# Kernel optimization log

Measured on AMD Instinct MI355X. Metric: run time of the kernel, lower is better.

## Reference

```python
import jax, jax.numpy as jnp
import numpy as np

B, T, D, V, M, K = 16, 4096, 512, 32000, 256, 3
OPERATOR_RANK = 8
COVERAGE_FLOOR = 0.05
LN_EPS = 1e-5


def _causal_conv(h, w, b):
    # h: [B,T,D] -> NCH layout, left-pad K-1 for causality (matches F.pad((pad,0)))
    x = h.transpose(0, 2, 1)
    k = w.shape[-1]
    y = jax.lax.conv_general_dilated(x, w, (1,), [(k - 1, 0)],
                                     dimension_numbers=('NCH', 'OIH', 'NCH'))
    return (y + b[None, :, None]).transpose(0, 2, 1)


def _layernorm(x, g, b):
    mu = x.mean(-1, keepdims=True)
    var = ((x - mu) ** 2).mean(-1, keepdims=True)
    return (x - mu) * jax.lax.rsqrt(var + LN_EPS) * g + b


def _masked_median(vals, mask):
    # torch .median() on n valid elems = sorted[(n-1)//2] (lower median)
    valid = mask > 0.5
    cnt = valid.sum(-1)  # [B]
    s = jnp.sort(jnp.where(valid, vals, jnp.inf), axis=-1)
    idx = jnp.maximum((cnt - 1) // 2, 0).astype(jnp.int32)
    med = jnp.take_along_axis(s, idx[:, None], axis=-1)  # [B,1]
    return jnp.where(cnt[:, None] > 0, med, 0.0)


def setup_inputs() -> dict:
    key = jax.random.key(0)
    ks = jax.random.split(key, 10)
    return {
        'prompt_content_units': jax.random.randint(ks[0], (B, T), 0, V),
        'prompt_duration_obs': jax.random.uniform(ks[1], (B, T), minval=0.01, maxval=1.0),
        'prompt_mask': (jax.random.uniform(ks[2], (B, T)) < 0.9).astype(jnp.float32),
        'emb': jax.random.normal(ks[3], (V, D)) * 0.02,
        'proj_w': jax.random.normal(ks[4], (D, 4)) * 0.1,
        'proj_b': jnp.zeros((D,)),
        'conv1_w': jax.random.normal(ks[5], (D, D, K)) * 0.02,
        'conv1_b': jnp.zeros((D,)),
        'conv2_w': jax.random.normal(ks[6], (D, D, K)) * 0.02,
        'conv2_b': jnp.zeros((D,)),
        'ln_g': jnp.ones((D,)),
        'ln_b': jnp.zeros((D,)),
        'role_key': jax.random.normal(ks[7], (M, D)) * 0.02,
    }


def reference(prompt_content_units, prompt_duration_obs, prompt_mask,
              emb, proj_w, proj_b, conv1_w, conv1_b, conv2_w, conv2_b,
              ln_g, ln_b, role_key):
    mask = jnp.clip(prompt_mask, 0.0, 1.0)                       # [B,T]
    logdur = jnp.log(jnp.maximum(prompt_duration_obs, 1e-4)) * mask
    z = jnp.zeros_like(logdur)
    aux = jnp.stack([logdur, z, z, z], axis=-1)                  # [B,T,4]
    hidden = emb[prompt_content_units] + aux @ proj_w.T + proj_b # [B,T,D]
    hidden = jax.nn.gelu(_causal_conv(hidden, conv1_w, conv1_b), approximate=False)
    hidden = jax.nn.gelu(_causal_conv(hidden, conv2_w, conv2_b), approximate=False)
    hidden = _layernorm(hidden, ln_g, ln_b) * mask[..., None]

    score = jnp.einsum('btd,md->btm', hidden, role_key) / jnp.sqrt(jnp.float32(D))
    score = jnp.where(mask[..., None] <= 0.0, -10000.0, score)
    attn = jax.nn.softmax(score, axis=-1) * mask[..., None]      # [B,T,M]

    support = jnp.maximum(mask.sum(1, keepdims=True), 1.0)       # [B,1]
    global_rate = _masked_median(logdur, mask)                   # [B,1]
    ref_residual = (logdur - global_rate) * mask                 # [B,T]

    coverage = jnp.maximum(attn.sum(1), 1e-6)                    # [B,M]
    role_value = jnp.einsum('btm,bt->bm', attn, ref_residual) / coverage
    diff2 = (ref_residual[..., None] - role_value[:, None, :]) ** 2
    role_var = jnp.maximum((attn * diff2).sum(1) / coverage, 1e-4)
    role_cov = jnp.maximum(coverage / support, COVERAGE_FLOOR)
    prompt_role_fit = jnp.einsum('btm,bm->bt', attn, role_value) * mask
    zero_operator = jnp.zeros((mask.shape[0], OPERATOR_RANK), dtype=prompt_duration_obs.dtype)

    return (global_rate, zero_operator, role_value, role_var, role_cov,
            mask, logdur, ref_residual, attn, prompt_role_fit)
```

## Files before the change

### kernel.cpp

```cpp
#include <hip/hip_runtime.h>
#include <math.h>
#include <stdint.h>

#define B_  16
#define T_  4096
#define D_  512
#define M_  256
#define TP_ 4098

static constexpr long O_RATE = 0;
static constexpr long O_ZOP  = 16;
static constexpr long O_RVAL = 144;
static constexpr long O_RVAR = 4240;
static constexpr long O_RCOV = 8336;
static constexpr long O_MASK = 12432;
static constexpr long O_LOGD = 77968;
static constexpr long O_RESID= 143504;
static constexpr long O_ATTN = 209040;
static constexpr long O_FIT  = 16986256;

typedef unsigned short u16;
typedef unsigned int u32;
typedef __attribute__((ext_vector_type(8))) __bf16 bf16x8;
typedef __attribute__((ext_vector_type(4))) float fx4;

__device__ __forceinline__ float b2f(u16 u){ union{float f;uint32_t i;}v; v.i=((uint32_t)u)<<16; return v.f; }
__device__ __forceinline__ u16 f2b(float f){ union{float f;uint32_t i;}v; v.f=f; uint32_t r=v.i+0x7fffu+((v.i>>16)&1u); return (u16)(r>>16); }
__device__ __forceinline__ float clip01(float x){ return fminf(fmaxf(x, 0.f), 1.f); }
__device__ __forceinline__ float gelu_f(float x){ return 0.5f*x*(1.0f+erff(x*0.70710678118654752440f)); }

__device__ __forceinline__ void cp16(const u16* g, u16* l){
  __builtin_amdgcn_global_load_lds((__attribute__((address_space(1))) void*)g,
                                   (__attribute__((address_space(3))) void*)l, 16, 0, 0);
}


__global__ void k_init(u16* __restrict__ h0, u16* __restrict__ hA, int Cloc,
                       float* __restrict__ out){
  int i = blockIdx.x*256 + threadIdx.x;
  int nA = Cloc << 7;
  if (i < nA){
    int lb = i >> 7, r = i & 127, g = r >> 1, t = r & 1;
    *(uint4*)(h0 + ((long)(lb*64 + g)*TP_ + t)*8) = make_uint4(0,0,0,0);
  } else if (i < nA + 2048){
    int j = i - nA;
    int b = j >> 7, r = j & 127, g = r >> 1, t = r & 1;
    *(uint4*)(hA + ((long)(b*64 + g)*TP_ + t)*8) = make_uint4(0,0,0,0);
  } else if (i < nA + 2048 + 128){
    out[O_ZOP + (i - nA - 2048)] = 0.f;
  }
}

__global__ void k_repack(const float* __restrict__ w1, const float* __restrict__ w2,
                         const float* __restrict__ rk, const float* __restrict__ lng,
                         u16* __restrict__ wrp2, u16* __restrict__ rkb){
  int i = blockIdx.x*256 + threadIdx.x;
  if (i < 1572864){
    int gi = i >> 3, c7 = i & 7;
    int row = gi & 511;
    int g   = (gi >> 9) & 3;
    int kt  = (gi >> 11) & 15;
    int tg  = gi >> 15;
    int conv = tg / 3, tap = tg % 3;
    int ic = kt*32 + g*8 + c7;
    const float* w = conv ? w2 : w1;
    wrp2[i] = f2b(w[(row*512 + ic)*3 + tap]);
  } else {
    int j = i - 1572864;
    int gi = j >> 3, c7 = j & 7;
    int n  = gi & 255;
    int g  = (gi >> 8) & 3;
    int kt = gi >> 10;
    int k  = kt*32 + g*8 + c7;
    rkb[j] = f2b(rk[n*512 + k] * lng[k]);
  }
}

__global__ __launch_bounds__(64) void k_gbb(const float* __restrict__ rk,
                                            const float* __restrict__ lng,
                                            const float* __restrict__ lnb,
                                            float* __restrict__ GB,
                                            float* __restrict__ BeB){
  int n = blockIdx.x, lane = threadIdx.x;
  float sg = 0.f, sb = 0.f;
  #pragma unroll
  for (int j = 0; j < 8; ++j){
    int k = lane*8 + j;
    float kv = rk[(long)n*512 + k];
    sg += lng[k]*kv; sb += lnb[k]*kv;
  }
  #pragma unroll
  for (int d=1; d<64; d<<=1){ sg += __shfl_xor(sg, d); sb += __shfl_xor(sb, d); }
  if (lane == 0){ GB[n] = sg; BeB[n] = sb; }
}

__global__ __launch_bounds__(1024) void k_median(
    const float* __restrict__ dur, const float* __restrict__ msk,
    float* __restrict__ out, float* __restrict__ supp_f){
  __shared__ u32 keys[4096];
  __shared__ u32 hist[2048];
  __shared__ float sred[1024];
  __shared__ u32 selBin, selRank;
  __shared__ float sMed;
  const int tid = threadIdx.x;
  const int b = blockIdx.x;
  float msum = 0.f;
  for (int i = tid; i < 4096; i += 1024){
    int bt = (b << 12) + i;
    float m  = clip01(msk[bt]);
    float ld = logf(fmaxf(dur[bt], 1e-4f)) * m;
    out[O_MASK + bt] = m;
    out[O_LOGD + bt] = ld;
    u32 u = __float_as_uint(ld);
    u32 k = (u & 0x80000000u) ? ~u : (u | 0x80000000u);
    keys[i] = (m > 0.5f) ? k : 0xFFFFFFFFu;
    msum += m;
  }
  sred[tid] = msum;
  __syncthreads();
  for (int s = 512; s > 0; s >>= 1){
    if (tid < s) sred[tid] += sred[tid + s];
    __syncthreads();
  }
  float msumT = sred[0];
  int cnt = (int)(msumT + 0.5f);
  u32 prefix = 0;
  u32 r = (cnt > 0) ? (u32)((cnt - 1) >> 1) : 0u;
  if (cnt > 0){
    #pragma unroll
    for (int p = 0; p < 3; ++p){
      const int shift = (p==0) ? 21 : (p==1) ? 10 : 0;
      const int nb = (p==2) ? 1024 : 2048;
      const u32 himask = (p==0) ? 0u : (0xFFFFFFFFu << (shift + ((p==2)?10:11)));
      hist[tid] = 0u; hist[tid + 1024] = 0u;
      __syncthreads();
      for (int i = tid; i < 4096; i += 1024){
        u32 k = keys[i];
        if ((k & himask) == prefix)
          atomicAdd(&hist[(k >> shift) & (u32)(nb-1)], 1u);
      }
      __syncthreads();
      if (tid < 64){
        u32 lane = tid;
        u32 cum = 0;
        for (int chunk = 0; chunk < nb/64; ++chunk){
          u32 v = hist[chunk*64 + lane];
          u32 incl = v;
          #pragma unroll
          for (int d = 1; d < 64; d <<= 1){
            u32 o = __shfl_up(incl, d);
            if (lane >= (u32)d) incl += o;
          }
          u32 total = __shfl(incl, 63);
          if (r < cum + total){
            u32 excl = incl - v;
            bool hit = (r >= cum + excl) && (r < cum + excl + v);
            unsigned long long bal = __ballot(hit);
            int L = __ffsll((unsigned long long)bal) - 1;
            u32 exclL = __shfl(excl, L);
            if (lane == 0){ selBin = (u32)(chunk*64 + L); selRank = r - (cum + exclL); }
            break;
          }
          cum += total;
        }
      }
      __syncthreads();
      prefix |= (selBin << shift);
      r = selRank;
      __syncthreads();
    }
  }
  if (tid == 0){
    float med = 0.f;
    if (cnt > 0){
      u32 k = prefix;
      u32 u = (k & 0x80000000u) ? (k ^ 0x80000000u) : ~k;
      med = __uint_as_float(u);
    }
    out[O_RATE + b] = med;
    supp_f[b] = fmaxf(msumT, 1.0f);
    sMed = med;
  }
  __syncthreads();
  float med = sMed;
  for (int i = tid; i < 4096; i += 1024){
    int bt = (b << 12) + i;
    float m  = clip01(msk[bt]);
    float ld = logf(fmaxf(dur[bt], 1e-4f)) * m;
    out[O_RESID + bt] = (ld - med) * m;
  }
}

__global__ __launch_bounds__(256) void k_embed(
    const int* __restrict__ units, const float* __restrict__ dur,
    const float* __restrict__ msk, const float* __restrict__ emb,
    const float* __restrict__ pw, const float* __restrict__ pb,
    u16* __restrict__ h0, int b0){
  int wid = threadIdx.x >> 6, lane = threadIdx.x & 63;
  int w = blockIdx.x*4 + wid;
  int tb = w & 63, g = (w >> 6) & 63, lb = w >> 12;
  int t = tb*64 + lane;
  int bt = ((b0 + lb) << 12) + t;
  float m = clip01(msk[bt]);
  float ld = logf(fmaxf(dur[bt], 1e-4f)) * m;
  long u = units[bt];
  const float* er = emb + u*512 + g*8;
  float4 e0 = *(const float4*)er;
  float4 e1 = *(const float4*)(er + 4);
  float x[8] = {e0.x,e0.y,e0.z,e0.w,e1.x,e1.y,e1.z,e1.w};
  union { u16 s[8]; uint4 v; } o;
  #pragma unroll
  for (int j=0;j<8;++j)
    o.s[j] = f2b(x[j] + ld*pw[(g*8+j)*4] + pb[g*8+j]);
  *(uint4*)(h0 + ((long)(lb*64 + g)*TP_ + 2 + t)*8) = o.v;
}

__device__ __forceinline__ void stageA(u16* smem, const u16* hin, long aG, int t0,
                                       int tid, int kt, int base){
  #pragma unroll
  for (int q = 0; q < 2; ++q){
    int s = q*512 + tid;
    int gl = s / 258, row = s - gl*258;
    cp16(hin + (aG + (long)(kt*4 + gl)*TP_ + t0 + row)*8, &smem[(base + s)*8]);
  }
  if (tid < 8){
    int s = 1024 + tid;
    cp16(hin + (aG + (long)(kt*4 + 3)*TP_ + t0 + (s - 774))*8, &smem[(base + s)*8]);
  }
}
__device__ __forceinline__ void stageB(u16* smem, const u16* w, int n0,
                                       int tid, int kt, int base){
  #pragma unroll
  for (int q = 0; q < 6; ++q){
    int s2 = q*512 + tid;
    int tap = s2 >> 10, g = (s2 >> 8) & 3, col = s2 & 255;
    cp16(w + ((long)((tap*16 + kt)*4 + g)*512 + n0 + col)*8, &smem[(base + s2)*8]);
  }
}

template<int STATS>
__global__ __launch_bounds__(512, 2) void k_conv(const u16* __restrict__ hin,
                                                 const u16* __restrict__ wrp2c,
                                                 const float* __restrict__ bias,
                                                 u16* __restrict__ hout,
                                                 float* __restrict__ rsum,
                                                 float* __restrict__ rsumsq,
                                                 int statsBase, int nwg){
  __shared__ __align__(16) u16 smem[65664];
  const int tid = threadIdx.x;
  const int lane = tid & 63, wid = tid >> 6;
  const int wm = wid >> 2, wn = wid & 3;
  const int g4 = lane >> 4, r16 = lane & 15;
  const int cpx = nwg >> 3;
  const int wg  = ((int)blockIdx.x & 7)*cpx + ((int)blockIdx.x >> 3);
  const int nt = wg & 1, mt = wg >> 1;
  const int lb = mt >> 4, t0 = (mt & 15) << 8;
  const int n0 = nt << 8;
  const long aG = (long)lb*64*TP_;

  fx4 acc[8][4];
  #pragma unroll
  for (int i=0;i<8;++i)
    #pragma unroll
    for (int j=0;j<4;++j){ acc[i][j][0]=0.f; acc[i][j][1]=0.f; acc[i][j][2]=0.f; acc[i][j][3]=0.f; }

  stageB(smem, wrp2c, n0, tid, 0, 2064);
  stageA(smem, hin, aG, t0, tid, 0, 0);

  int cur = 0;
  #pragma unroll 1
  for (int kt = 0; kt < 16; ++kt){
    if (kt < 15){
      stageB(smem, wrp2c, n0, tid, kt+1, 2064 + (cur^1)*3072);
      stageA(smem, hin, aG, t0, tid, kt+1, (cur^1)*1032);
      asm volatile("s_waitcnt vmcnt(8)" ::: "memory");
    } else {
      asm volatile("s_waitcnt vmcnt(0)" ::: "memory");
    }
    __builtin_amdgcn_s_barrier();
    __builtin_amdgcn_sched_barrier(0);
    {
      const u16* Ab = &smem[cur*1032*8];
      const u16* Bb = &smem[(2064 + cur*3072)*8];
      #pragma unroll
      for (int tap = 0; tap < 3; ++tap){
        bf16x8 af[8], bf[4];
        #pragma unroll
        for (int mi=0;mi<8;++mi)
          af[mi] = *(const bf16x8*)&Ab[(g4*258 + wm*128 + mi*16 + r16 + tap)*8];
        #pragma unroll
        for (int ni=0;ni<4;++ni)
          bf[ni] = *(const bf16x8*)&Bb[(tap*1024 + g4*256 + wn*64 + ni*16 + r16)*8];
        __builtin_amdgcn_s_setprio(1);
        #pragma unroll
        for (int mi=0;mi<8;++mi)
          #pragma unroll
          for (int ni=0;ni<4;++ni)
            acc[mi][ni] = __builtin_amdgcn_mfma_f32_16x16x32_bf16(af[mi], bf[ni], acc[mi][ni], 0,0,0);
        __builtin_amdgcn_s_setprio(0);
      }
    }
    __builtin_amdgcn_sched_barrier(0);
    __builtin_amdgcn_s_barrier();
    cur ^= 1;
  }

  __builtin_amdgcn_sched_barrier(0);
  const int cl = r16;
  float bv[4];
  #pragma unroll
  for (int ni=0;ni<4;++ni) bv[ni] = bias[n0 + wn*64 + ni*16 + cl];
  #pragma unroll
  for (int mi=0;mi<8;++mi)
    #pragma unroll
    for (int rg=0;rg<4;++rg){
      int r = wm*128 + mi*16 + g4*4 + rg;
      float sv = 0.f, sv2 = 0.f;
      #pragma unroll
      for (int ni=0;ni<4;++ni){
        float v = gelu_f(acc[mi][ni][rg] + bv[ni]);
        int c = wn*64 + ni*16 + cl;
        smem[(c >> 3)*2048 + r*8 + (c & 7)] = f2b(v);
        if (STATS){ sv += v; sv2 += v*v; }
      }
      if (STATS){
        #pragma unroll
        for (int d=1; d<16; d<<=1){ sv += __shfl_xor(sv, d); sv2 += __shfl_xor(sv2, d); }
        if (cl == 0){
          int grow = statsBase + lb*4096 + t0 + r;
          atomicAdd(&rsum[grow], sv);
          atomicAdd(&rsumsq[grow], sv2);
        }
      }
    }
  __syncthreads();
  #pragma unroll
  for (int it = 0; it < 16; ++it){
    int s = it*512 + tid;
    int gc = s >> 8, row = s & 255;
    long gran = aG + (long)(nt*32 + gc)*TP_ + 2 + t0 + row;
    *(uint4*)(hout + gran*8) = *(const uint4*)&smem[gc*2048 + row*8];
  }
}

__global__ __launch_bounds__(256, 2) void k_score(const u16* __restrict__ h,
                                                  const u16* __restrict__ rkb,
                                                  const float* __restrict__ msk,
                                                  const float* __restrict__ rsum,
                                                  const float* __restrict__ rsumsq,
                                                  const float* __restrict__ GB,
                                                  const float* __restrict__ BeB,
                                                  float* __restrict__ S0,
                                                  float* __restrict__ S1,
                                                  float* __restrict__ S2,
                                                  float* __restrict__ out, int b0){
  __shared__ __align__(16) u16 smem[12288];
  __shared__ float smax[128][2];
  __shared__ float ssum[128][2];
  const int tid = threadIdx.x;
  const int lane = tid & 63, wid = tid >> 6;
  const int wm = wid >> 1, wn = wid & 1;
  const int r0 = blockIdx.x << 7;
  const int lb = r0 >> 12, t0 = r0 & 4095;
  const int gb = b0 + lb;
  const long gRow0 = ((long)gb << 12) + t0;
  const long aG = (long)lb*64*TP_;
  const int g4 = lane >> 4, r16 = lane & 15;

  fx4 acc[4][8];
  #pragma unroll
  for (int i=0;i<4;++i)
    #pragma unroll
    for (int j=0;j<8;++j){ acc[i][j][0]=0.f; acc[i][j][1]=0.f; acc[i][j][2]=0.f; acc[i][j][3]=0.f; }

  for (int kt = 0; kt < 16; ++kt){
    #pragma unroll
    for (int q = 0; q < 2; ++q){
      int s = q*256 + tid;
      int gl = s >> 7, row = s & 127;
      cp16(h + (aG + (long)(kt*4 + gl)*TP_ + 2 + t0 + row)*8, &smem[s*8]);
    }
    #pragma unroll
    for (int q = 0; q < 4; ++q){
      int s2 = q*256 + tid;
      cp16(rkb + ((long)kt*1024 + s2)*8, &smem[(512 + s2)*8]);
    }
    __syncthreads();
    bf16x8 af[4], bf[8];
    #pragma unroll
    for (int mi=0;mi<4;++mi)
      af[mi] = *(const bf16x8*)&smem[(g4*128 + wm*64 + mi*16 + r16)*8];
    #pragma unroll
    for (int ni=0;ni<8;++ni)
      bf[ni] = *(const bf16x8*)&smem[(512 + g4*256 + wn*128 + ni*16 + r16)*8];
    #pragma unroll
    for (int mi=0;mi<4;++mi)
      #pragma unroll
      for (int ni=0;ni<8;++ni)
        acc[mi][ni] = __builtin_amdgcn_mfma_f32_16x16x32_bf16(af[mi], bf[ni], acc[mi][ni], 0,0,0);
    __syncthreads();
  }
  const float SCALE = 0.044194173824159216f;
  const int cl = r16;
  float gbv[8], bbv[8];
  #pragma unroll
  for (int ni=0;ni<8;++ni){
    int col = wn*128 + ni*16 + cl;
    gbv[ni] = GB[col]; bbv[ni] = BeB[col];
  }
  float gmx[4][4];
  #pragma unroll
  for (int mi=0;mi<4;++mi)
    #pragma unroll
    for (int rg=0;rg<4;++rg){
      int row = wm*64 + mi*16 + g4*4 + rg;
      long gRow = gRow0 + row;
      float mk = clip01(msk[gRow]);
      float mu = rsum[gRow] * (1.f/512.f);
      float var = rsumsq[gRow] * (1.f/512.f) - mu*mu;
      float inv = rsqrtf(var + 1e-5f);
      float mx = -1e30f;
      #pragma unroll
      for (int ni=0;ni<8;++ni){
        float s = mk * SCALE * (inv*(acc[mi][ni][rg] - mu*gbv[ni]) + bbv[ni]);
        acc[mi][ni][rg] = s;
        mx = fmaxf(mx, s);
      }
      #pragma unroll
      for (int d=1; d<16; d<<=1) mx = fmaxf(mx, __shfl_xor(mx, d));
      if (cl == 0) smax[row][wn] = mx;
    }
  __syncthreads();
  #pragma unroll
  for (int mi=0;mi<4;++mi)
    #pragma unroll
    for (int rg=0;rg<4;++rg){
      int row = wm*64 + mi*16 + g4*4 + rg;
      gmx[mi][rg] = fmaxf(smax[row][0], smax[row][1]);
    }
  #pragma unroll
  for (int mi=0;mi<4;++mi)
    #pragma unroll
    for (int rg=0;rg<4;++rg){
      float s = 0.f;
      #pragma unroll
      for (int ni=0;ni<8;++ni){
        float e = expf(acc[mi][ni][rg] - gmx[mi][rg]);
        acc[mi][ni][rg] = e;
        s += e;
      }
      #pragma unroll
      for (int d=1; d<16; d<<=1) s += __shfl_xor(s, d);
      if (cl == 0) ssum[wm*64 + mi*16 + g4*4 + rg][wn] = s;
    }
  __syncthreads();
  float ps0[8], ps1[8], ps2[8];
  #pragma unroll
  for (int ni=0;ni<8;++ni){ ps0[ni]=0.f; ps1[ni]=0.f; ps2[ni]=0.f; }
  #pragma unroll
  for (int mi=0;mi<4;++mi)
    #pragma unroll
    for (int rg=0;rg<4;++rg){
      int row = wm*64 + mi*16 + g4*4 + rg;
      long gRow = gRow0 + row;
      float tot = ssum[row][0] + ssum[row][1];
      float mk = clip01(msk[gRow]);
      float f = mk / tot;
      float rr = out[O_RESID + gRow];
      #pragma unroll
      for (int ni=0;ni<8;++ni){
        float a = acc[mi][ni][rg] * f;
        out[O_ATTN + gRow*M_ + wn*128 + ni*16 + cl] = a;
        ps0[ni] += a; ps1[ni] += a*rr; ps2[ni] += a*rr*rr;
      }
    }
  #pragma unroll
  for (int ni=0;ni<8;++ni){
    ps0[ni] += __shfl_xor(ps0[ni], 16); ps0[ni] += __shfl_xor(ps0[ni], 32);
    ps1[ni] += __shfl_xor(ps1[ni], 16); ps1[ni] += __shfl_xor(ps1[ni], 32);
    ps2[ni] += __shfl_xor(ps2[ni], 16); ps2[ni] += __shfl_xor(ps2[ni], 32);
  }
  if (g4 == 0){
    #pragma unroll
    for (int ni=0;ni<8;++ni){
      int col = wn*128 + ni*16 + cl;
      atomicAdd(&S0[gb*M_ + col], ps0[ni]);
      atomicAdd(&S1[gb*M_ + col], ps1[ni]);
      atomicAdd(&S2[gb*M_ + col], ps2[ni]);
    }
  }
}

__global__ __launch_bounds__(256) void k_final(const float* __restrict__ S0,
                                               const float* __restrict__ S1,
                                               const float* __restrict__ S2,
                                               const float* __restrict__ supp,
                                               float* __restrict__ out,
                                               float* __restrict__ rvf){
  int i = blockIdx.x*256 + threadIdx.x;
  int b = i >> 8;
  float s0 = S0[i], s1 = S1[i], s2 = S2[i];
  float cov = fmaxf(s0, 1e-6f);
  float rv = s1 / cov;
  float var = fmaxf((s2 - 2.f*rv*s1 + rv*rv*s0) / cov, 1e-4f);
  float rc = fmaxf(cov / supp[b], 0.05f);
  out[O_RVAL + i] = rv;
  out[O_RVAR + i] = var;
  out[O_RCOV + i] = rc;
  rvf[i] = rv;
}

__global__ __launch_bounds__(256) void k_fit(const float* __restrict__ attn,
                                             const float* __restrict__ rvf,
                                             const float* __restrict__ msk,
                                             float* __restrict__ out){
  int wid = threadIdx.x >> 6, lane = threadIdx.x & 63;
  int row = blockIdx.x*4 + wid;
  int b = row >> 12;
  float4 a = *(const float4*)(attn + (long)row*M_ + lane*4);
  float4 r = *(const float4*)(rvf + b*M_ + lane*4);
  float dot = a.x*r.x + a.y*r.y + a.z*r.z + a.w*r.w;
  #pragma unroll
  for (int d=1; d<64; d<<=1) dot += __shfl_xor(dot, d);
  if (lane == 0) out[O_FIT + row] = dot * clip01(msk[row]);
}

extern "C" void kernel_launch(void* const* d_in, const int* in_sizes, int n_in,
                              void* d_out, int out_size, void* d_ws, size_t ws_size,
                              hipStream_t stream) {
  const int*   units = (const int*)d_in[0];
  const float* dur   = (const float*)d_in[1];
  const float* msk   = (const float*)d_in[2];
  const float* emb   = (const float*)d_in[3];
  const float* pw    = (const float*)d_in[4];
  const float* pb    = (const float*)d_in[5];
  const float* w1    = (const float*)d_in[6];
  const float* b1    = (const float*)d_in[7];
  const float* w2    = (const float*)d_in[8];
  const float* b2c   = (const float*)d_in[9];
  const float* lng   = (const float*)d_in[10];
  const float* lnb   = (const float*)d_in[11];
  const float* rk    = (const float*)d_in[12];
  float* out = (float*)d_out;
  char* ws = (char*)d_ws;

  u16* hA = (u16*)(out + O_ATTN);

  const size_t perB = (size_t)64*TP_*16;
  const size_t tail = 3145728 + 262144 + 1024 + 1024 + 64 + 16384 + 49152 + 262144 + 262144;
  int C = 16;
  while (C > 1 && ((size_t)C*perB + tail) > ws_size) C >>= 1;
  const int nch = 16 / C;

  char* p = ws;
  u16*   h0    = (u16*)p;            p += (size_t)C*perB;
  u16*   wrp2  = (u16*)p;            p += 3145728;
  u16*   rkb   = (u16*)p;            p += 262144;
  float* GB    = (float*)p;          p += 1024;
  float* BeB   = (float*)p;          p += 1024;
  float* supp_f= (float*)p;          p += 64;
  float* rv_f  = (float*)p;          p += 16384;
  float* S0    = (float*)p;          p += 49152;
  float* S1    = S0 + 4096;
  float* S2    = S1 + 4096;
  float* rsum  = (float*)p;          p += 262144;
  float* rsumsq= (float*)p;          p += 262144;

  hipMemsetAsync(S0, 0, 49152 + 262144 + 262144, stream);
  int initN = (C << 7) + 2048 + 128;
  k_init  <<<(initN + 255)/256, 256, 0, stream>>>(h0, hA, C, out);
  k_repack<<<6656, 256, 0, stream>>>(w1, w2, rk, lng, wrp2, rkb);
  k_gbb   <<<256,   64, 0, stream>>>(rk, lng, lnb, GB, BeB);
  k_median<<<16,  1024, 0, stream>>>(dur, msk, out, supp_f);
  const int nwg = C*32;
  for (int c = 0; c < nch; ++c){
    int b0 = c*C;
    u16* hAc = hA + (size_t)b0*64*TP_*8;
    k_embed  <<<C*1024, 256, 0, stream>>>(units, dur, msk, emb, pw, pb, h0, b0);
    k_conv<0><<<nwg,    512, 0, stream>>>(h0,  wrp2,           b1,  hAc, rsum, rsumsq, 0,       nwg);
    k_conv<1><<<nwg,    512, 0, stream>>>(hAc, wrp2 + 786432,  b2c, h0,  rsum, rsumsq, b0*4096, nwg);
    k_score  <<<C*32,   256, 0, stream>>>(h0, rkb, msk, rsum, rsumsq, GB, BeB, S0, S1, S2, out, b0);
  }
  k_final <<<16,    256, 0, stream>>>(S0, S1, S2, supp_f, out, rv_f);
  k_fit   <<<16384, 256, 0, stream>>>(out + O_ATTN, rv_f, msk, out);
}
```

Before: 499.4 us.

## Interleave per-tap weight prefetch with split half-tile MFMA phases in conv kernel

Restructures the conv GEMM main loop so each k-step is split into six phases: per tap and per half of the M rows, fragments are loaded from LDS, the next k-step's A tile and per-tap B tile are issued as async copies, and MFMAs run between barriers. Weight staging is spread across the iteration instead of issued in one burst, and fragment registers are halved (4 A fragments instead of 8). The aim is better overlap of global-to-LDS copies with MFMA work and lower register pressure. In exchange it adds many more barriers and hand-tuned vmcnt waits, which could cost synchronisation overhead or race if the counts are wrong.

```diff
diff --git a/kernel.cpp b/kernel.cpp
--- a/kernel.cpp
+++ b/kernel.cpp
@@ -216,26 +216,59 @@
 }
 
 __device__ __forceinline__ void stageA(u16* smem, const u16* hin, long aG, int t0,
-                                       int tid, int kt, int base){
+                                       int tid, int kt, int slotbase){
   #pragma unroll
   for (int q = 0; q < 2; ++q){
     int s = q*512 + tid;
     int gl = s / 258, row = s - gl*258;
-    cp16(hin + (aG + (long)(kt*4 + gl)*TP_ + t0 + row)*8, &smem[(base + s)*8]);
+    cp16(hin + (aG + (long)(kt*4 + gl)*TP_ + t0 + row)*8, &smem[(slotbase + s)*8]);
   }
   if (tid < 8){
     int s = 1024 + tid;
-    cp16(hin + (aG + (long)(kt*4 + 3)*TP_ + t0 + (s - 774))*8, &smem[(base + s)*8]);
-  }
-}
-__device__ __forceinline__ void stageB(u16* smem, const u16* w, int n0,
-                                       int tid, int kt, int base){
-  #pragma unroll
-  for (int q = 0; q < 6; ++q){
-    int s2 = q*512 + tid;
-    int tap = s2 >> 10, g = (s2 >> 8) & 3, col = s2 & 255;
-    cp16(w + ((long)((tap*16 + kt)*4 + g)*512 + n0 + col)*8, &smem[(base + s2)*8]);
-  }
+    cp16(hin + (aG + (long)(kt*4 + 3)*TP_ + t0 + (s - 774))*8, &smem[(slotbase + s)*8]);
+  }
+}
+__device__ __forceinline__ void stageBt(u16* smem, const u16* w, int n0,
+                                        int tid, int kt, int tap, int slotbase){
+  #pragma unroll
+  for (int q = 0; q < 2; ++q){
+    int s = q*512 + tid;
+    int g = s >> 8, col = s & 255;
+    cp16(w + ((long)((tap*16 + kt)*4 + g)*512 + n0 + col)*8, &smem[(slotbase + s)*8]);
+  }
+}
+
+template<int H>
+__device__ __forceinline__ void conv_tail(bf16x8 af[4], bf16x8 bf[4], fx4 acc[8][4]){
+  __builtin_amdgcn_s_barrier();
+  asm volatile("s_waitcnt lgkmcnt(0)" ::: "memory");
+  __builtin_amdgcn_sched_barrier(0);
+  __builtin_amdgcn_s_setprio(1);
+  #pragma unroll
+  for (int mi=0;mi<4;++mi)
+    #pragma unroll
+    for (int ni=0;ni<4;++ni)
+      acc[H*4+mi][ni] = __builtin_amdgcn_mfma_f32_16x16x32_bf16(af[mi], bf[ni], acc[H*4+mi][ni], 0,0,0);
+  __builtin_amdgcn_s_setprio(0);
+  __builtin_amdgcn_sched_barrier(0);
+  __builtin_amdgcn_s_barrier();
+}
+
+template<int T>
+__device__ __forceinline__ void loadB(bf16x8 bf[4], const u16* smem, int cur,
+                                      int g4, int r16, int wn){
+  const u16* Bb = &smem[(2064 + T*2048 + cur*1024)*8];
+  #pragma unroll
+  for (int ni=0;ni<4;++ni)
+    bf[ni] = *(const bf16x8*)&Bb[(g4*256 + wn*64 + ni*16 + r16)*8];
+}
+template<int T, int H>
+__device__ __forceinline__ void loadA(bf16x8 af[4], const u16* smem, int cur,
+                                      int g4, int r16, int wm){
+  const u16* Ab = &smem[(cur*1032)*8];
+  #pragma unroll
+  for (int mi=0;mi<4;++mi)
+    af[mi] = *(const bf16x8*)&Ab[(g4*258 + wm*128 + (H*4+mi)*16 + r16 + T)*8];
 }
 
 template<int STATS>
@@ -264,45 +297,50 @@
     #pragma unroll
     for (int j=0;j<4;++j){ acc[i][j][0]=0.f; acc[i][j][1]=0.f; acc[i][j][2]=0.f; acc[i][j][3]=0.f; }
 
-  stageB(smem, wrp2c, n0, tid, 0, 2064);
-  stageA(smem, hin, aG, t0, tid, 0, 0);
-
-  int cur = 0;
+  stageA (smem, hin, aG, t0, tid, 0, 0);
+  stageBt(smem, wrp2c, n0, tid, 0, 0, 2064);
+  stageBt(smem, wrp2c, n0, tid, 0, 1, 2064 + 2048);
+  stageBt(smem, wrp2c, n0, tid, 0, 2, 2064 + 4096);
+  asm volatile("s_waitcnt vmcnt(4)" ::: "memory");
+  __builtin_amdgcn_s_barrier();
+
   #pragma unroll 1
   for (int kt = 0; kt < 16; ++kt){
-    if (kt < 15){
-      stageB(smem, wrp2c, n0, tid, kt+1, 2064 + (cur^1)*3072);
-      stageA(smem, hin, aG, t0, tid, kt+1, (cur^1)*1032);
-      asm volatile("s_waitcnt vmcnt(8)" ::: "memory");
-    } else {
-      asm volatile("s_waitcnt vmcnt(0)" ::: "memory");
-    }
-    __builtin_amdgcn_s_barrier();
-    __builtin_amdgcn_sched_barrier(0);
-    {
-      const u16* Ab = &smem[cur*1032*8];
-      const u16* Bb = &smem[(2064 + cur*3072)*8];
-      #pragma unroll
-      for (int tap = 0; tap < 3; ++tap){
-        bf16x8 af[8], bf[4];
-        #pragma unroll
-        for (int mi=0;mi<8;++mi)
-          af[mi] = *(const bf16x8*)&Ab[(g4*258 + wm*128 + mi*16 + r16 + tap)*8];
-        #pragma unroll
-        for (int ni=0;ni<4;++ni)
-          bf[ni] = *(const bf16x8*)&Bb[(tap*1024 + g4*256 + wn*64 + ni*16 + r16)*8];
-        __builtin_amdgcn_s_setprio(1);
-        #pragma unroll
-        for (int mi=0;mi<8;++mi)
-          #pragma unroll
-          for (int ni=0;ni<4;++ni)
-            acc[mi][ni] = __builtin_amdgcn_mfma_f32_16x16x32_bf16(af[mi], bf[ni], acc[mi][ni], 0,0,0);
-        __builtin_amdgcn_s_setprio(0);
-      }
-    }
-    __builtin_amdgcn_sched_barrier(0);
-    __builtin_amdgcn_s_barrier();
-    cur ^= 1;
+    const int cur = kt & 1, nxt = cur ^ 1;
+    const bool pf = (kt < 15);
+    bf16x8 af[4], bf[4];
+
+    loadB<0>(bf, smem, cur, g4, r16, wn);
+    loadA<0,0>(af, smem, cur, g4, r16, wm);
+    if (pf){
+      stageA (smem, hin, aG, t0, tid, kt+1, nxt*1032);
+      stageBt(smem, wrp2c, n0, tid, kt+1, 0, 2064 + nxt*1024);
+    }
+    conv_tail<0>(af, bf, acc);
+
+    loadA<0,1>(af, smem, cur, g4, r16, wm);
+    if (pf) asm volatile("s_waitcnt vmcnt(6)" ::: "memory");
+    else    asm volatile("s_waitcnt vmcnt(2)" ::: "memory");
+    conv_tail<1>(af, bf, acc);
+
+    loadB<1>(bf, smem, cur, g4, r16, wn);
+    loadA<1,0>(af, smem, cur, g4, r16, wm);
+    if (pf) stageBt(smem, wrp2c, n0, tid, kt+1, 1, 2064 + 2048 + nxt*1024);
+    conv_tail<0>(af, bf, acc);
+
+    loadA<1,1>(af, smem, cur, g4, r16, wm);
+    if (pf) asm volatile("s_waitcnt vmcnt(6)" ::: "memory");
+    else    asm volatile("s_waitcnt vmcnt(0)" ::: "memory");
+    conv_tail<1>(af, bf, acc);
+
+    loadB<2>(bf, smem, cur, g4, r16, wn);
+    loadA<2,0>(af, smem, cur, g4, r16, wm);
+    if (pf) stageBt(smem, wrp2c, n0, tid, kt+1, 2, 2064 + 4096 + nxt*1024);
+    conv_tail<0>(af, bf, acc);
+
+    loadA<2,1>(af, smem, cur, g4, r16, wm);
+    if (pf) asm volatile("s_waitcnt vmcnt(4)" ::: "memory");
+    conv_tail<1>(af, bf, acc);
   }
 
   __builtin_amdgcn_sched_barrier(0);
```

Result: no change. 504.5 us (+1.0%).

## Restructure conv GEMM: 128-row tiles, A fragments from global, 4-slot B pipeline

Applied to the files above, without the earlier changes.

The causal conv kernel now uses 256-thread workgroups on 128x256 output tiles, doubling the grid. Activation (A) fragments are loaded straight from global memory into registers and double-buffered across phases, replacing the LDS staging. Only the weights (B) go through a 4-slot shared-memory ring, with per-tap phases unrolled by templates. This cuts LDS footprint and barrier-heavy staging, at the cost of uncoalesced, redundant global reads of A across waves and more per-phase barriers.

```diff
diff --git a/kernel.cpp b/kernel.cpp
--- a/kernel.cpp
+++ b/kernel.cpp
@@ -215,46 +215,92 @@
   *(uint4*)(h0 + ((long)(lb*64 + g)*TP_ + 2 + t)*8) = o.v;
 }
 
-__device__ __forceinline__ void stageA(u16* smem, const u16* hin, long aG, int t0,
-                                       int tid, int kt, int base){
-  #pragma unroll
-  for (int q = 0; q < 2; ++q){
-    int s = q*512 + tid;
-    int gl = s / 258, row = s - gl*258;
-    cp16(hin + (aG + (long)(kt*4 + gl)*TP_ + t0 + row)*8, &smem[(base + s)*8]);
-  }
-  if (tid < 8){
-    int s = 1024 + tid;
-    cp16(hin + (aG + (long)(kt*4 + 3)*TP_ + t0 + (s - 774))*8, &smem[(base + s)*8]);
-  }
-}
-__device__ __forceinline__ void stageB(u16* smem, const u16* w, int n0,
-                                       int tid, int kt, int base){
-  #pragma unroll
-  for (int q = 0; q < 6; ++q){
-    int s2 = q*512 + tid;
-    int tap = s2 >> 10, g = (s2 >> 8) & 3, col = s2 & 255;
-    cp16(w + ((long)((tap*16 + kt)*4 + g)*512 + n0 + col)*8, &smem[(base + s2)*8]);
-  }
+__device__ __forceinline__ void ldA(bf16x8 af[8], const u16* __restrict__ hin,
+                                    long aG, int t0, int kt, int tap,
+                                    int g4, int r16){
+  const u16* pA = hin + (aG + (long)(kt*4 + g4)*TP_ + t0 + r16 + tap)*8;
+  #pragma unroll
+  for (int mi=0;mi<8;++mi)
+    af[mi] = *(const bf16x8*)(pA + mi*256);
+}
+__device__ __forceinline__ void stB(u16* smem, const u16* __restrict__ w, int n0,
+                                    int tid, int kt, int tap, int slot){
+  #pragma unroll
+  for (int q=0;q<4;++q){
+    int s = q*256 + tid;
+    cp16(w + ((long)((tap*16 + kt)*4 + (s>>8))*512 + n0 + (s&255))*8,
+         &smem[(slot*1024 + s)*8]);
+  }
+}
+
+template<bool TAIL, int I>
+__device__ __forceinline__ void phase(int kt0, u16* smem,
+    const u16* __restrict__ hin, const u16* __restrict__ wrp2c,
+    long aG, int t0, int n0, int tid,
+    bf16x8 afC[8], bf16x8 afN[8], fx4 acc[8][4], int wn, int g4, int r16){
+  __builtin_amdgcn_s_barrier();
+  if (TAIL && I >= 10) asm volatile("s_waitcnt vmcnt(0)" ::: "memory");
+  else                 asm volatile("s_waitcnt vmcnt(4)" ::: "memory");
+  __builtin_amdgcn_sched_barrier(0);
+  if (!TAIL || I <= 10)
+    ldA(afN, hin, aG, t0, kt0 + (I+1)/3, (I+1)%3, g4, r16);
+  if (!TAIL || I <= 8)
+    stB(smem, wrp2c, n0, tid, kt0 + 1 + I/3, I%3, (I+3)&3);
+  bf16x8 bf[4];
+  {
+    const u16* Bb = &smem[((I&3)*1024)*8];
+    #pragma unroll
+    for (int ni=0;ni<4;++ni)
+      bf[ni] = *(const bf16x8*)&Bb[(g4*256 + wn*64 + ni*16 + r16)*8];
+  }
+  asm volatile("s_waitcnt lgkmcnt(0)" ::: "memory");
+  __builtin_amdgcn_sched_barrier(0);
+  __builtin_amdgcn_s_setprio(1);
+  #pragma unroll
+  for (int mi=0;mi<8;++mi)
+    #pragma unroll
+    for (int ni=0;ni<4;++ni)
+      acc[mi][ni] = __builtin_amdgcn_mfma_f32_16x16x32_bf16(afC[mi], bf[ni], acc[mi][ni], 0,0,0);
+  __builtin_amdgcn_s_setprio(0);
+  __builtin_amdgcn_sched_barrier(0);
+}
+
+template<bool TAIL>
+__device__ __forceinline__ void run12(int kt0, u16* smem,
+    const u16* __restrict__ hin, const u16* __restrict__ wrp2c,
+    long aG, int t0, int n0, int tid,
+    bf16x8 af0[8], bf16x8 af1[8], fx4 acc[8][4], int wn, int g4, int r16){
+  phase<TAIL,0 >(kt0, smem, hin, wrp2c, aG, t0, n0, tid, af0, af1, acc, wn, g4, r16);
+  phase<TAIL,1 >(kt0, smem, hin, wrp2c, aG, t0, n0, tid, af1, af0, acc, wn, g4, r16);
+  phase<TAIL,2 >(kt0, smem, hin, wrp2c, aG, t0, n0, tid, af0, af1, acc, wn, g4, r16);
+  phase<TAIL,3 >(kt0, smem, hin, wrp2c, aG, t0, n0, tid, af1, af0, acc, wn, g4, r16);
+  phase<TAIL,4 >(kt0, smem, hin, wrp2c, aG, t0, n0, tid, af0, af1, acc, wn, g4, r16);
+  phase<TAIL,5 >(kt0, smem, hin, wrp2c, aG, t0, n0, tid, af1, af0, acc, wn, g4, r16);
+  phase<TAIL,6 >(kt0, smem, hin, wrp2c, aG, t0, n0, tid, af0, af1, acc, wn, g4, r16);
+  phase<TAIL,7 >(kt0, smem, hin, wrp2c, aG, t0, n0, tid, af1, af0, acc, wn, g4, r16);
+  phase<TAIL,8 >(kt0, smem, hin, wrp2c, aG, t0, n0, tid, af0, af1, acc, wn, g4, r16);
+  phase<TAIL,9 >(kt0, smem, hin, wrp2c, aG, t0, n0, tid, af1, af0, acc, wn, g4, r16);
+  phase<TAIL,10>(kt0, smem, hin, wrp2c, aG, t0, n0, tid, af0, af1, acc, wn, g4, r16);
+  phase<TAIL,11>(kt0, smem, hin, wrp2c, aG, t0, n0, tid, af1, af0, acc, wn, g4, r16);
 }
 
 template<int STATS>
-__global__ __launch_bounds__(512, 2) void k_conv(const u16* __restrict__ hin,
+__global__ __launch_bounds__(256, 2) void k_conv(const u16* __restrict__ hin,
                                                  const u16* __restrict__ wrp2c,
                                                  const float* __restrict__ bias,
                                                  u16* __restrict__ hout,
                                                  float* __restrict__ rsum,
                                                  float* __restrict__ rsumsq,
                                                  int statsBase, int nwg){
-  __shared__ __align__(16) u16 smem[65664];
+  __shared__ __align__(16) u16 smem[32768];
   const int tid = threadIdx.x;
   const int lane = tid & 63, wid = tid >> 6;
-  const int wm = wid >> 2, wn = wid & 3;
+  const int wn = wid;
   const int g4 = lane >> 4, r16 = lane & 15;
   const int cpx = nwg >> 3;
   const int wg  = ((int)blockIdx.x & 7)*cpx + ((int)blockIdx.x >> 3);
   const int nt = wg & 1, mt = wg >> 1;
-  const int lb = mt >> 4, t0 = (mt & 15) << 8;
+  const int lb = mt >> 5, t0 = (mt & 31) << 7;
   const int n0 = nt << 8;
   const long aG = (long)lb*64*TP_;
 
@@ -264,48 +310,18 @@
     #pragma unroll
     for (int j=0;j<4;++j){ acc[i][j][0]=0.f; acc[i][j][1]=0.f; acc[i][j][2]=0.f; acc[i][j][3]=0.f; }
 
-  stageB(smem, wrp2c, n0, tid, 0, 2064);
-  stageA(smem, hin, aG, t0, tid, 0, 0);
-
-  int cur = 0;
+  bf16x8 af0[8], af1[8];
+  stB(smem, wrp2c, n0, tid, 0, 0, 0);
+  stB(smem, wrp2c, n0, tid, 0, 1, 1);
+  ldA(af0, hin, aG, t0, 0, 0, g4, r16);
+  stB(smem, wrp2c, n0, tid, 0, 2, 2);
+
   #pragma unroll 1
-  for (int kt = 0; kt < 16; ++kt){
-    if (kt < 15){
-      stageB(smem, wrp2c, n0, tid, kt+1, 2064 + (cur^1)*3072);
-      stageA(smem, hin, aG, t0, tid, kt+1, (cur^1)*1032);
-      asm volatile("s_waitcnt vmcnt(8)" ::: "memory");
-    } else {
-      asm volatile("s_waitcnt vmcnt(0)" ::: "memory");
-    }
-    __builtin_amdgcn_s_barrier();
-    __builtin_amdgcn_sched_barrier(0);
-    {
-      const u16* Ab = &smem[cur*1032*8];
-      const u16* Bb = &smem[(2064 + cur*3072)*8];
-      #pragma unroll
-      for (int tap = 0; tap < 3; ++tap){
-        bf16x8 af[8], bf[4];
-        #pragma unroll
-        for (int mi=0;mi<8;++mi)
-          af[mi] = *(const bf16x8*)&Ab[(g4*258 + wm*128 + mi*16 + r16 + tap)*8];
-        #pragma unroll
-        for (int ni=0;ni<4;++ni)
-          bf[ni] = *(const bf16x8*)&Bb[(tap*1024 + g4*256 + wn*64 + ni*16 + r16)*8];
-        __builtin_amdgcn_s_setprio(1);
-        #pragma unroll
-        for (int mi=0;mi<8;++mi)
-          #pragma unroll
-          for (int ni=0;ni<4;++ni)
-            acc[mi][ni] = __builtin_amdgcn_mfma_f32_16x16x32_bf16(af[mi], bf[ni], acc[mi][ni], 0,0,0);
-        __builtin_amdgcn_s_setprio(0);
-      }
-    }
-    __builtin_amdgcn_sched_barrier(0);
-    __builtin_amdgcn_s_barrier();
-    cur ^= 1;
-  }
-
-  __builtin_amdgcn_sched_barrier(0);
+  for (int kt0 = 0; kt0 < 12; kt0 += 4)
+    run12<false>(kt0, smem, hin, wrp2c, aG, t0, n0, tid, af0, af1, acc, wn, g4, r16);
+  run12<true>(12, smem, hin, wrp2c, aG, t0, n0, tid, af0, af1, acc, wn, g4, r16);
+
+  __syncthreads();
   const int cl = r16;
   float bv[4];
   #pragma unroll
@@ -314,13 +330,13 @@
   for (int mi=0;mi<8;++mi)
     #pragma unroll
     for (int rg=0;rg<4;++rg){
-      int r = wm*128 + mi*16 + g4*4 + rg;
+      int r = mi*16 + g4*4 + rg;
       float sv = 0.f, sv2 = 0.f;
       #pragma unroll
       for (int ni=0;ni<4;++ni){
         float v = gelu_f(acc[mi][ni][rg] + bv[ni]);
         int c = wn*64 + ni*16 + cl;
-        smem[(c >> 3)*2048 + r*8 + (c & 7)] = f2b(v);
+        smem[(c >> 3)*1024 + r*8 + (c & 7)] = f2b(v);
         if (STATS){ sv += v; sv2 += v*v; }
       }
       if (STATS){
@@ -336,10 +352,10 @@
   __syncthreads();
   #pragma unroll
   for (int it = 0; it < 16; ++it){
-    int s = it*512 + tid;
-    int gc = s >> 8, row = s & 255;
+    int s = it*256 + tid;
+    int gc = s >> 7, row = s & 127;
     long gran = aG + (long)(nt*32 + gc)*TP_ + 2 + t0 + row;
-    *(uint4*)(hout + gran*8) = *(const uint4*)&smem[gc*2048 + row*8];
+    *(uint4*)(hout + gran*8) = *(const uint4*)&smem[(gc*128 + row)*8];
   }
 }
 
@@ -572,13 +588,13 @@
   k_repack<<<6656, 256, 0, stream>>>(w1, w2, rk, lng, wrp2, rkb);
   k_gbb   <<<256,   64, 0, stream>>>(rk, lng, lnb, GB, BeB);
   k_median<<<16,  1024, 0, stream>>>(dur, msk, out, supp_f);
-  const int nwg = C*32;
+  const int nwg = C*64;
   for (int c = 0; c < nch; ++c){
     int b0 = c*C;
     u16* hAc = hA + (size_t)b0*64*TP_*8;
     k_embed  <<<C*1024, 256, 0, stream>>>(units, dur, msk, emb, pw, pb, h0, b0);
-    k_conv<0><<<nwg,    512, 0, stream>>>(h0,  wrp2,           b1,  hAc, rsum, rsumsq, 0,       nwg);
-    k_conv<1><<<nwg,    512, 0, stream>>>(hAc, wrp2 + 786432,  b2c, h0,  rsum, rsumsq, b0*4096, nwg);
+    k_conv<0><<<nwg,    256, 0, stream>>>(h0,  wrp2,           b1,  hAc, rsum, rsumsq, 0,       nwg);
+    k_conv<1><<<nwg,    256, 0, stream>>>(hAc, wrp2 + 786432,  b2c, h0,  rsum, rsumsq, b0*4096, nwg);
     k_score  <<<C*32,   256, 0, stream>>>(h0, rkb, msk, rsum, rsumsq, GB, BeB, S0, S1, S2, out, b0);
   }
   k_final <<<16,    256, 0, stream>>>(S0, S1, S2, supp_f, out, rv_f);
```

After: 533.7 us. +6.9%, slower.

## Double-buffer score GEMM loads and split across 8 waves with block swizzle

Applied to the files above, without the earlier changes.

The score kernel now runs 512 threads (8 waves, 2x4 layout), so each wave holds a 64x64 tile instead of 64x128, which halves accumulator registers. Global-to-LDS copies of the next K slice are prefetched into a second buffer while MFMAs run on the current one, with explicit vmcnt waits and raw barriers. Block indices are remapped so neighbouring blocks fall into different groups of eight, and MFMA issue gets raised priority. The cost is twice the shared memory and softmax reductions across four column groups instead of two.

```diff
diff --git a/kernel.cpp b/kernel.cpp
--- a/kernel.cpp
+++ b/kernel.cpp
@@ -343,7 +343,7 @@
   }
 }
 
-__global__ __launch_bounds__(256, 2) void k_score(const u16* __restrict__ h,
+__global__ __launch_bounds__(512, 4) void k_score(const u16* __restrict__ h,
                                                   const u16* __restrict__ rkb,
                                                   const float* __restrict__ msk,
                                                   const float* __restrict__ rsum,
@@ -354,58 +354,79 @@
                                                   float* __restrict__ S1,
                                                   float* __restrict__ S2,
                                                   float* __restrict__ out, int b0){
-  __shared__ __align__(16) u16 smem[12288];
-  __shared__ float smax[128][2];
-  __shared__ float ssum[128][2];
+  __shared__ __align__(16) u16 smem[24576];
+  __shared__ float smax[128][4];
+  __shared__ float ssum[128][4];
   const int tid = threadIdx.x;
   const int lane = tid & 63, wid = tid >> 6;
-  const int wm = wid >> 1, wn = wid & 1;
-  const int r0 = blockIdx.x << 7;
+  const int wm = wid >> 2, wn = wid & 3;
+  const int g4 = lane >> 4, r16 = lane & 15;
+  const int cpx = (int)gridDim.x >> 3;
+  const int wg  = ((int)blockIdx.x & 7)*cpx + ((int)blockIdx.x >> 3);
+  const int r0 = wg << 7;
   const int lb = r0 >> 12, t0 = r0 & 4095;
   const int gb = b0 + lb;
   const long gRow0 = ((long)gb << 12) + t0;
   const long aG = (long)lb*64*TP_;
-  const int g4 = lane >> 4, r16 = lane & 15;
-
-  fx4 acc[4][8];
+
+  fx4 acc[4][4];
   #pragma unroll
   for (int i=0;i<4;++i)
     #pragma unroll
-    for (int j=0;j<8;++j){ acc[i][j][0]=0.f; acc[i][j][1]=0.f; acc[i][j][2]=0.f; acc[i][j][3]=0.f; }
-
+    for (int j=0;j<4;++j){ acc[i][j][0]=0.f; acc[i][j][1]=0.f; acc[i][j][2]=0.f; acc[i][j][3]=0.f; }
+
+  #define SC_STAGE(kt, buf) do {                                               \
+    int s = tid; int gl = s >> 7, row = s & 127;                               \
+    cp16(h + (aG + (long)((kt)*4 + gl)*TP_ + 2 + t0 + row)*8,                  \
+         &smem[((buf)*512 + s)*8]);                                            \
+    _Pragma("unroll")                                                          \
+    for (int q = 0; q < 2; ++q){                                               \
+      int s2 = q*512 + tid;                                                    \
+      cp16(rkb + ((long)(kt)*1024 + s2)*8,                                     \
+           &smem[(1024 + (buf)*1024 + s2)*8]);                                 \
+    } } while(0)
+
+  SC_STAGE(0, 0);
+  #pragma unroll 1
   for (int kt = 0; kt < 16; ++kt){
-    #pragma unroll
-    for (int q = 0; q < 2; ++q){
-      int s = q*256 + tid;
-      int gl = s >> 7, row = s & 127;
-      cp16(h + (aG + (long)(kt*4 + gl)*TP_ + 2 + t0 + row)*8, &smem[s*8]);
-    }
-    #pragma unroll
-    for (int q = 0; q < 4; ++q){
-      int s2 = q*256 + tid;
-      cp16(rkb + ((long)kt*1024 + s2)*8, &smem[(512 + s2)*8]);
-    }
-    __syncthreads();
-    bf16x8 af[4], bf[8];
-    #pragma unroll
-    for (int mi=0;mi<4;++mi)
-      af[mi] = *(const bf16x8*)&smem[(g4*128 + wm*64 + mi*16 + r16)*8];
-    #pragma unroll
-    for (int ni=0;ni<8;++ni)
-      bf[ni] = *(const bf16x8*)&smem[(512 + g4*256 + wn*128 + ni*16 + r16)*8];
-    #pragma unroll
-    for (int mi=0;mi<4;++mi)
-      #pragma unroll
-      for (int ni=0;ni<8;++ni)
-        acc[mi][ni] = __builtin_amdgcn_mfma_f32_16x16x32_bf16(af[mi], bf[ni], acc[mi][ni], 0,0,0);
-    __syncthreads();
-  }
+    const int cur = kt & 1;
+    if (kt < 15){
+      SC_STAGE(kt+1, cur^1);
+      asm volatile("s_waitcnt vmcnt(3)" ::: "memory");
+    } else {
+      asm volatile("s_waitcnt vmcnt(0)" ::: "memory");
+    }
+    __builtin_amdgcn_s_barrier();
+    __builtin_amdgcn_sched_barrier(0);
+    {
+      const u16* Ab = &smem[(cur*512)*8];
+      const u16* Bb = &smem[(1024 + cur*1024)*8];
+      bf16x8 af[4], bf[4];
+      #pragma unroll
+      for (int mi=0;mi<4;++mi)
+        af[mi] = *(const bf16x8*)&Ab[(g4*128 + wm*64 + mi*16 + r16)*8];
+      #pragma unroll
+      for (int ni=0;ni<4;++ni)
+        bf[ni] = *(const bf16x8*)&Bb[(g4*256 + wn*64 + ni*16 + r16)*8];
+      __builtin_amdgcn_s_setprio(1);
+      #pragma unroll
+      for (int mi=0;mi<4;++mi)
+        #pragma unroll
+        for (int ni=0;ni<4;++ni)
+          acc[mi][ni] = __builtin_amdgcn_mfma_f32_16x16x32_bf16(af[mi], bf[ni], acc[mi][ni], 0,0,0);
+      __builtin_amdgcn_s_setprio(0);
+    }
+    __builtin_amdgcn_sched_barrier(0);
+    __builtin_amdgcn_s_barrier();
+  }
+  #undef SC_STAGE
+
   const float SCALE = 0.044194173824159216f;
   const int cl = r16;
-  float gbv[8], bbv[8];
-  #pragma unroll
-  for (int ni=0;ni<8;++ni){
-    int col = wn*128 + ni*16 + cl;
+  float gbv[4], bbv[4];
+  #pragma unroll
+  for (int ni=0;ni<4;++ni){
+    int col = wn*64 + ni*16 + cl;
     gbv[ni] = GB[col]; bbv[ni] = BeB[col];
   }
   float gmx[4][4];
@@ -421,7 +442,7 @@
       float inv = rsqrtf(var + 1e-5f);
       float mx = -1e30f;
       #pragma unroll
-      for (int ni=0;ni<8;++ni){
+      for (int ni=0;ni<4;++ni){
         float s = mk * SCALE * (inv*(acc[mi][ni][rg] - mu*gbv[ni]) + bbv[ni]);
         acc[mi][ni][rg] = s;
         mx = fmaxf(mx, s);
@@ -436,7 +457,8 @@
     #pragma unroll
     for (int rg=0;rg<4;++rg){
       int row = wm*64 + mi*16 + g4*4 + rg;
-      gmx[mi][rg] = fmaxf(smax[row][0], smax[row][1]);
+      gmx[mi][rg] = fmaxf(fmaxf(smax[row][0], smax[row][1]),
+                          fmaxf(smax[row][2], smax[row][3]));
     }
   #pragma unroll
   for (int mi=0;mi<4;++mi)
@@ -444,7 +466,7 @@
     for (int rg=0;rg<4;++rg){
       float s = 0.f;
       #pragma unroll
-      for (int ni=0;ni<8;++ni){
+      for (int ni=0;ni<4;++ni){
         float e = expf(acc[mi][ni][rg] - gmx[mi][rg]);
         acc[mi][ni][rg] = e;
         s += e;
@@ -454,36 +476,36 @@
       if (cl == 0) ssum[wm*64 + mi*16 + g4*4 + rg][wn] = s;
     }
   __syncthreads();
-  float ps0[8], ps1[8], ps2[8];
-  #pragma unroll
-  for (int ni=0;ni<8;++ni){ ps0[ni]=0.f; ps1[ni]=0.f; ps2[ni]=0.f; }
+  float ps0[4], ps1[4], ps2[4];
+  #pragma unroll
+  for (int ni=0;ni<4;++ni){ ps0[ni]=0.f; ps1[ni]=0.f; ps2[ni]=0.f; }
   #pragma unroll
   for (int mi=0;mi<4;++mi)
     #pragma unroll
     for (int rg=0;rg<4;++rg){
       int row = wm*64 + mi*16 + g4*4 + rg;
       long gRow = gRow0 + row;
-      float tot = ssum[row][0] + ssum[row][1];
+      float tot = (ssum[row][0] + ssum[row][1]) + (ssum[row][2] + ssum[row][3]);
       float mk = clip01(msk[gRow]);
       float f = mk / tot;
       float rr = out[O_RESID + gRow];
       #pragma unroll
-      for (int ni=0;ni<8;++ni){
+      for (int ni=0;ni<4;++ni){
         float a = acc[mi][ni][rg] * f;
-        out[O_ATTN + gRow*M_ + wn*128 + ni*16 + cl] = a;
+        out[O_ATTN + gRow*M_ + wn*64 + ni*16 + cl] = a;
         ps0[ni] += a; ps1[ni] += a*rr; ps2[ni] += a*rr*rr;
       }
     }
   #pragma unroll
-  for (int ni=0;ni<8;++ni){
+  for (int ni=0;ni<4;++ni){
     ps0[ni] += __shfl_xor(ps0[ni], 16); ps0[ni] += __shfl_xor(ps0[ni], 32);
     ps1[ni] += __shfl_xor(ps1[ni], 16); ps1[ni] += __shfl_xor(ps1[ni], 32);
     ps2[ni] += __shfl_xor(ps2[ni], 16); ps2[ni] += __shfl_xor(ps2[ni], 32);
   }
   if (g4 == 0){
     #pragma unroll
-    for (int ni=0;ni<8;++ni){
-      int col = wn*128 + ni*16 + cl;
+    for (int ni=0;ni<4;++ni){
+      int col = wn*64 + ni*16 + cl;
       atomicAdd(&S0[gb*M_ + col], ps0[ni]);
       atomicAdd(&S1[gb*M_ + col], ps1[ni]);
       atomicAdd(&S2[gb*M_ + col], ps2[ni]);
@@ -579,7 +601,7 @@
     k_embed  <<<C*1024, 256, 0, stream>>>(units, dur, msk, emb, pw, pb, h0, b0);
     k_conv<0><<<nwg,    512, 0, stream>>>(h0,  wrp2,           b1,  hAc, rsum, rsumsq, 0,       nwg);
     k_conv<1><<<nwg,    512, 0, stream>>>(hAc, wrp2 + 786432,  b2c, h0,  rsum, rsumsq, b0*4096, nwg);
-    k_score  <<<C*32,   256, 0, stream>>>(h0, rkb, msk, rsum, rsumsq, GB, BeB, S0, S1, S2, out, b0);
+    k_score  <<<C*32,   512, 0, stream>>>(h0, rkb, msk, rsum, rsumsq, GB, BeB, S0, S1, S2, out, b0);
   }
   k_final <<<16,    256, 0, stream>>>(S0, S1, S2, supp_f, out, rv_f);
   k_fit   <<<16384, 256, 0, stream>>>(out + O_ATTN, rv_f, msk, out);
```

New measurement: 502.1 us. No clear change (+0.5%).
